# Performance work log

Hardware: AMD Instinct MI355X
Metric: run time of the kernel (lower is better)

## Reference

```python
import jax, jax.numpy as jnp
import numpy as np

DIM = 1024
DIM_HEAD = 64
HEADS = 8
MULT = 4
ATTN_INNER = HEADS * DIM_HEAD            # 512
FF_INNER = MULT * DIM                    # 4096
FUSED = ATTN_INNER + DIM_HEAD + DIM_HEAD + 2 * FF_INNER  # 8832


def setup_inputs() -> dict:
    key = jax.random.key(0)
    ks = jax.random.split(key, 5)
    x = jax.random.normal(ks[0], (2, 2048, DIM), dtype=jnp.float32)
    gamma = jnp.ones((DIM,), dtype=jnp.float32)
    # Linear weights stored as [in, out]
    w_fused = jax.random.normal(ks[1], (DIM, FUSED), dtype=jnp.float32) * (DIM ** -0.5)
    w_attn_out = jax.random.normal(ks[2], (ATTN_INNER, DIM), dtype=jnp.float32) * (ATTN_INNER ** -0.5)
    w_ff_out = jax.random.normal(ks[3], (FF_INNER, DIM), dtype=jnp.float32) * (FF_INNER ** -0.5)
    return {"x": x, "gamma": gamma, "w_fused": w_fused,
            "w_attn_out": w_attn_out, "w_ff_out": w_ff_out}


def _forward(x, gamma, w_fused, w_attn_out, w_ff_out):
    b, n, d = x.shape
    # LayerNorm (beta buffer is zeros)
    mu = jnp.mean(x, axis=-1, keepdims=True)
    var = jnp.mean(jnp.square(x - mu), axis=-1, keepdims=True)
    xn = (x - mu) * jax.lax.rsqrt(var + 1e-5) * gamma
    # fused QKV + FF projection
    proj = jnp.einsum('bnd,df->bnf', xn, w_fused)
    q = proj[..., :ATTN_INNER]
    k = proj[..., ATTN_INNER:ATTN_INNER + DIM_HEAD]
    v = proj[..., ATTN_INNER + DIM_HEAD:ATTN_INNER + 2 * DIM_HEAD]
    ff = proj[..., ATTN_INNER + 2 * DIM_HEAD:]
    # multi-query attention: single shared K/V head of width DIM_HEAD
    q = q.reshape(b, n, HEADS, DIM_HEAD).transpose(0, 2, 1, 3) * (DIM_HEAD ** -0.5)
    sim = jnp.einsum('bhid,bjd->bhij', q, k)
    attn = jax.nn.softmax(sim, axis=-1)
    out = jnp.einsum('bhij,bjd->bhid', attn, v)
    out = out.transpose(0, 2, 1, 3).reshape(b, n, ATTN_INNER)
    attn_out = jnp.einsum('bna,ad->bnd', out, w_attn_out)
    # parallel SwiGLU FF: chunk -> (x_part, gate); silu(gate)*x_part
    ff_x, gate = ff[..., :FF_INNER], ff[..., FF_INNER:]
    ff_out = jnp.einsum('bnf,fd->bnd', jax.nn.silu(gate) * ff_x, w_ff_out)
    return attn_out + ff_out


def reference(x, gamma, w_fused, w_attn_out, w_ff_out):
    return _forward(x, gamma, w_fused, w_attn_out, w_ff_out)
```

## Files before the change

### kernel.cpp

```cpp
#include <hip/hip_runtime.h>
#include <hip/hip_bf16.h>
#include <stdint.h>

#define DIM     1024
#define SEQ     2048
#define NTOK    4096
#define HEADS   8
#define DH      64
#define AINNER  512
#define FFI     4096
#define FUSED   8832
#define HCOLS   4608

typedef __attribute__((ext_vector_type(8))) short short8;
typedef __attribute__((ext_vector_type(4))) short short4v;
typedef __attribute__((ext_vector_type(4))) float f32x4;

__device__ __forceinline__ short f2bf(float f) {
  union { float f; uint32_t u; } v; v.f = f;
  uint32_t r = v.u + 0x7fffu + ((v.u >> 16) & 1u);
  return (short)(r >> 16);
}
__device__ __forceinline__ float bf2f(short s) {
  union { uint32_t u; float f; } v; v.u = ((uint32_t)(uint16_t)s) << 16;
  return v.f;
}
__device__ __forceinline__ void g2l16(const void* g, void* l) {
  __builtin_amdgcn_global_load_lds((const __attribute__((address_space(1))) void*)g,
                                   (__attribute__((address_space(3))) void*)l, 16, 0, 0);
}

__global__ __launch_bounds__(256) void k_transpose_wf(const float* __restrict__ src,
                                                      short* __restrict__ dst) {
  __shared__ short tile[32][33];
  int c0 = blockIdx.x * 32;
  int r0 = blockIdx.y * 32;
  int tx = threadIdx.x & 31, ty = threadIdx.x >> 5;
#pragma unroll
  for (int i = 0; i < 32; i += 8)
    tile[ty + i][tx] = f2bf(src[(size_t)(r0 + ty + i) * FUSED + c0 + tx]);
  __syncthreads();
#pragma unroll
  for (int i = 0; i < 32; i += 8)
    dst[(size_t)(c0 + ty + i) * DIM + r0 + tx] = tile[tx][ty + i];
}

__global__ __launch_bounds__(256) void k_transpose_w2(const float* __restrict__ wao,
                                                      const float* __restrict__ wfo,
                                                      short* __restrict__ dst) {
  __shared__ short tile[32][33];
  int c0 = blockIdx.x * 32;
  int r0 = blockIdx.y * 32;
  int tx = threadIdx.x & 31, ty = threadIdx.x >> 5;
#pragma unroll
  for (int i = 0; i < 32; i += 8) {
    int r = r0 + ty + i;
    float v = (r < AINNER) ? wao[(size_t)r * DIM + c0 + tx]
                           : wfo[(size_t)(r - AINNER) * DIM + c0 + tx];
    tile[ty + i][tx] = f2bf(v);
  }
  __syncthreads();
#pragma unroll
  for (int i = 0; i < 32; i += 8)
    dst[(size_t)(c0 + ty + i) * HCOLS + r0 + tx] = tile[tx][ty + i];
}

__global__ __launch_bounds__(256) void k_ln(const float* __restrict__ x,
                                            const float* __restrict__ gamma,
                                            short* __restrict__ xn) {
  int row = blockIdx.x;
  int t = threadIdx.x;
  const float4* xr = (const float4*)(x + (size_t)row * DIM);
  float4 v = xr[t];
  float s = v.x + v.y + v.z + v.w;
  float s2 = v.x * v.x + v.y * v.y + v.z * v.z + v.w * v.w;
#pragma unroll
  for (int m = 1; m < 64; m <<= 1) { s += __shfl_xor(s, m); s2 += __shfl_xor(s2, m); }
  __shared__ float red[8];
  int w = t >> 6;
  if ((t & 63) == 0) { red[w] = s; red[4 + w] = s2; }
  __syncthreads();
  s = red[0] + red[1] + red[2] + red[3];
  s2 = red[4] + red[5] + red[6] + red[7];
  float mu = s * (1.f / DIM);
  float rs = rsqrtf(s2 * (1.f / DIM) - mu * mu + 1e-5f);
  const float4* g4 = (const float4*)gamma;
  float4 g = g4[t];
  short4v o;
  o.x = f2bf((v.x - mu) * rs * g.x);
  o.y = f2bf((v.y - mu) * rs * g.y);
  o.z = f2bf((v.z - mu) * rs * g.z);
  o.w = f2bf((v.w - mu) * rs * g.w);
  ((short4v*)(xn + (size_t)row * DIM))[t] = o;
}

__global__ __launch_bounds__(512, 2) void p1(const short* __restrict__ A,
                                             const short* __restrict__ Bt,
                                             short* __restrict__ qb,
                                             short* __restrict__ kbf,
                                             short* __restrict__ vtb,
                                             short* __restrict__ H) {
  extern __shared__ __align__(16) short S[];
  int tid = threadIdx.x, l = tid & 63, w = tid >> 6;
  int wm = w >> 2, wn = w & 3;
  int hw = blockIdx.y * 37 + blockIdx.x;
  int tile = (hw & 7) * 74 + (hw >> 3);
  int bx = tile % 37, by = tile / 37;
  int mBase = by * 256;
  bool fused = bx < 32;
  int b0row = fused ? (640 + bx * 128) : ((bx - 32) * 128);
  int b1row = 4736 + bx * 128;

  int srow = w * 8 + (l >> 3);
  int cs = (l & 7) ^ (l >> 3);
  const short* Ag = A + (size_t)(mBase + srow) * DIM + cs * 8;
  const short* Bg0 = Bt + (size_t)(b0row + srow) * DIM + cs * 8;
  const short* Bg1 = Bt + (size_t)(b1row + srow) * DIM + cs * 8;
  int dsto = w * 512 + l * 8;

#define P1_STAGE(kt, db)                                                        \
  {                                                                             \
    _Pragma("unroll") for (int i = 0; i < 4; ++i)                               \
        g2l16(Ag + (size_t)(i * 64) * DIM + (kt) * 64,                          \
              S + (db) * 16384 + i * 4096 + dsto);                              \
    _Pragma("unroll") for (int i = 0; i < 2; ++i)                               \
        g2l16(Bg0 + (size_t)(i * 64) * DIM + (kt) * 64,                         \
              S + 32768 + (db) * 16384 + i * 4096 + dsto);                      \
    if (fused) {                                                                \
      _Pragma("unroll") for (int i = 0; i < 2; ++i)                             \
          g2l16(Bg1 + (size_t)(i * 64) * DIM + (kt) * 64,                       \
                S + 32768 + (db) * 16384 + 8192 + i * 4096 + dsto);             \
    }                                                                           \
  }

  const int NT = DIM / 64;
  P1_STAGE(0, 0);

  int c0 = l & 15, kg = l >> 4, cx = l & 7;
  f32x4 zero = {0.f, 0.f, 0.f, 0.f};
  f32x4 accF[8][2], accG[8][2];
#pragma unroll
  for (int m = 0; m < 8; ++m)
#pragma unroll
    for (int n = 0; n < 2; ++n) { accF[m][n] = zero; accG[m][n] = zero; }

  for (int kt = 0; kt < NT; ++kt) {
    int db = kt & 1, dbn = db ^ 1;
    asm volatile("s_waitcnt vmcnt(0)\ns_barrier" ::: "memory");
    if (kt + 1 < NT) P1_STAGE(kt + 1, dbn);
    const short* Ab = S + db * 16384;
    const short* Bb = S + 32768 + db * 16384;
#pragma unroll
    for (int kkh = 0; kkh < 2; ++kkh) {
      int ch8 = ((kkh * 4 + kg) ^ cx) * 8;
      short8 bf0 = *(const short8*)(Bb + (wn * 32 + c0) * 64 + ch8);
      short8 bf1 = *(const short8*)(Bb + (wn * 32 + 16 + c0) * 64 + ch8);
      if (fused) {
        short8 bg0 = *(const short8*)(Bb + (128 + wn * 32 + c0) * 64 + ch8);
        short8 bg1 = *(const short8*)(Bb + (128 + wn * 32 + 16 + c0) * 64 + ch8);
        __builtin_amdgcn_s_setprio(1);
#pragma unroll
        for (int m = 0; m < 8; ++m) {
          short8 a = *(const short8*)(Ab + (wm * 128 + m * 16 + c0) * 64 + ch8);
          accF[m][0] = __builtin_amdgcn_mfma_f32_16x16x32_bf16(a, bf0, accF[m][0], 0, 0, 0);
          accF[m][1] = __builtin_amdgcn_mfma_f32_16x16x32_bf16(a, bf1, accF[m][1], 0, 0, 0);
          accG[m][0] = __builtin_amdgcn_mfma_f32_16x16x32_bf16(a, bg0, accG[m][0], 0, 0, 0);
          accG[m][1] = __builtin_amdgcn_mfma_f32_16x16x32_bf16(a, bg1, accG[m][1], 0, 0, 0);
        }
        __builtin_amdgcn_s_setprio(0);
      } else {
        __builtin_amdgcn_s_setprio(1);
#pragma unroll
        for (int m = 0; m < 8; ++m) {
          short8 a = *(const short8*)(Ab + (wm * 128 + m * 16 + c0) * 64 + ch8);
          accF[m][0] = __builtin_amdgcn_mfma_f32_16x16x32_bf16(a, bf0, accF[m][0], 0, 0, 0);
          accF[m][1] = __builtin_amdgcn_mfma_f32_16x16x32_bf16(a, bf1, accF[m][1], 0, 0, 0);
        }
        __builtin_amdgcn_s_setprio(0);
      }
    }
  }
#undef P1_STAGE

  int r0 = (l >> 4) * 4;
#pragma unroll
  for (int m = 0; m < 8; ++m)
#pragma unroll
    for (int n = 0; n < 2; ++n)
#pragma unroll
      for (int r = 0; r < 4; ++r) {
        int row = mBase + wm * 128 + m * 16 + r0 + r;
        if (fused) {
          int col = bx * 128 + wn * 32 + n * 16 + c0;
          float g = accG[m][n][r];
          float sg = g / (1.f + __expf(-g));
          H[(size_t)row * HCOLS + AINNER + col] = f2bf(sg * accF[m][n][r]);
        } else {
          int col = (bx - 32) * 128 + wn * 32 + n * 16 + c0;
          float val = accF[m][n][r];
          if (col < AINNER)
            qb[(size_t)row * AINNER + col] = f2bf(val);
          else if (col < AINNER + DH)
            kbf[(size_t)row * DH + (col - AINNER)] = f2bf(val);
          else
            vtb[((size_t)(row >> 11) * DH + (col - AINNER - DH)) * SEQ +
                (row & (SEQ - 1))] = f2bf(val);
        }
      }
}

__global__ __launch_bounds__(512, 2) void gemm_s(const short* __restrict__ A,
                                                 const short* __restrict__ Bt,
                                                 short* __restrict__ part) {
  extern __shared__ __align__(16) short S[];
  int tid = threadIdx.x, l = tid & 63, w = tid >> 6;
  int wm = w >> 2, wn = w & 3;
  int hw = (blockIdx.z * 16 + blockIdx.y) * 4 + blockIdx.x;
  int tile = (hw & 7) * 32 + (hw >> 3);
  int bx = tile & 3, by = (tile >> 2) & 15, bz = tile >> 6;
  int mBase = by * 256, nBase = bx * 256;
  int kOff = bz * 1152;

  int srow = w * 8 + (l >> 3);
  int cs = (l & 7) ^ (l >> 3);
  const short* Ag = A + (size_t)(mBase + srow) * HCOLS + kOff + cs * 8;
  const short* Bg = Bt + (size_t)(nBase + srow) * HCOLS + kOff + cs * 8;
  int dsto = w * 512 + l * 8;

#define GS_STAGE(kt, db)                                                        \
  {                                                                             \
    _Pragma("unroll") for (int i = 0; i < 4; ++i) {                             \
      g2l16(Ag + (size_t)(i * 64) * HCOLS + (kt) * 64,                          \
            S + (db) * 16384 + i * 4096 + dsto);                                \
      g2l16(Bg + (size_t)(i * 64) * HCOLS + (kt) * 64,                          \
            S + 32768 + (db) * 16384 + i * 4096 + dsto);                        \
    }                                                                           \
  }

  const int NT = 18;
  GS_STAGE(0, 0);

  int c0 = l & 15, kg = l >> 4, cx = l & 7;
  f32x4 zero = {0.f, 0.f, 0.f, 0.f};
  f32x4 acc[8][4];
#pragma unroll
  for (int m = 0; m < 8; ++m)
#pragma unroll
    for (int n = 0; n < 4; ++n) acc[m][n] = zero;

  for (int kt = 0; kt < NT; ++kt) {
    int db = kt & 1, dbn = db ^ 1;
    asm volatile("s_waitcnt vmcnt(0)\ns_barrier" ::: "memory");
    if (kt + 1 < NT) GS_STAGE(kt + 1, dbn);
    const short* Ab = S + db * 16384;
    const short* Bb = S + 32768 + db * 16384;
#pragma unroll
    for (int kkh = 0; kkh < 2; ++kkh) {
      int ch8 = ((kkh * 4 + kg) ^ cx) * 8;
      short8 b[4];
#pragma unroll
      for (int n = 0; n < 4; ++n)
        b[n] = *(const short8*)(Bb + (wn * 64 + n * 16 + c0) * 64 + ch8);
      __builtin_amdgcn_s_setprio(1);
#pragma unroll
      for (int m = 0; m < 8; ++m) {
        short8 a = *(const short8*)(Ab + (wm * 128 + m * 16 + c0) * 64 + ch8);
#pragma unroll
        for (int n = 0; n < 4; ++n)
          acc[m][n] = __builtin_amdgcn_mfma_f32_16x16x32_bf16(a, b[n], acc[m][n], 0, 0, 0);
      }
      __builtin_amdgcn_s_setprio(0);
    }
  }
#undef GS_STAGE

  int r0 = (l >> 4) * 4;
#pragma unroll
  for (int m = 0; m < 8; ++m)
#pragma unroll
    for (int n = 0; n < 4; ++n)
#pragma unroll
      for (int r = 0; r < 4; ++r) {
        int row = mBase + wm * 128 + m * 16 + r0 + r;
        int col = nBase + wn * 64 + n * 16 + c0;
        part[(size_t)bz * (NTOK * DIM) + (size_t)row * DIM + col] = f2bf(acc[m][n][r]);
      }
}

__global__ __launch_bounds__(256) void k_red(const short* __restrict__ part,
                                             float* __restrict__ out) {
  int i = (blockIdx.x * 256 + threadIdx.x) * 4;
  float4 s = {0.f, 0.f, 0.f, 0.f};
#pragma unroll
  for (int ks = 0; ks < 4; ++ks) {
    short4v v = *(const short4v*)(part + (size_t)ks * (NTOK * DIM) + i);
    s.x += bf2f(v.x); s.y += bf2f(v.y); s.z += bf2f(v.z); s.w += bf2f(v.w);
  }
  *(float4*)(out + i) = s;
}

__global__ __launch_bounds__(512, 2) void gemm_r(const short* __restrict__ A, int lda,
                                                 const short* __restrict__ Bt, int ldb,
                                                 int K, float* __restrict__ out0) {
  extern __shared__ __align__(16) short SA[];
  int tid = threadIdx.x, l = tid & 63, w = tid >> 6;
  int gx = gridDim.x;
  int nwg = gx * gridDim.y;
  int hw = blockIdx.y * gx + blockIdx.x;
  int qq = nwg >> 3;
  int tile = (hw & 7) * qq + (hw >> 3);
  int bx = tile % gx, by = tile / gx;
  int mBase = by * 128, nBase = bx * 128;

  int srow = w * 8 + (l >> 3);
  int cs = (l & 7) ^ (l >> 3);
  const short* Ag = A + (size_t)(mBase + srow) * lda + cs * 8;
  const short* Bg = Bt + (size_t)(nBase + srow) * ldb + cs * 8;
  short* ldsA = SA + w * 512 + l * 8;
  short* ldsB = ldsA + 8192;

  int NT = K >> 6;
  for (int tt = 0; tt < 3; ++tt) {
    int slot = tt & 3;
#pragma unroll
    for (int i = 0; i < 2; ++i) {
      g2l16(Ag + (size_t)(i * 64) * lda + tt * 64, ldsA + slot * 16384 + i * 4096);
      g2l16(Bg + (size_t)(i * 64) * ldb + tt * 64, ldsB + slot * 16384 + i * 4096);
    }
  }

  int wr = w >> 2, wc = w & 3;
  int c0 = l & 15, kg = l >> 4, cx = l & 7;
  f32x4 zero = {0.f, 0.f, 0.f, 0.f};
  f32x4 acc[4][2];
#pragma unroll
  for (int m = 0; m < 4; ++m)
#pragma unroll
    for (int n = 0; n < 2; ++n) acc[m][n] = zero;

  for (int kt = 0; kt < NT; ++kt) {
    if (kt + 2 < NT)      asm volatile("s_waitcnt vmcnt(8)\ns_barrier" ::: "memory");
    else if (kt + 1 < NT) asm volatile("s_waitcnt vmcnt(4)\ns_barrier" ::: "memory");
    else                  asm volatile("s_waitcnt vmcnt(0)\ns_barrier" ::: "memory");
    int slot = kt & 3;
    const short* Ab = SA + slot * 16384;
    const short* Bb = Ab + 8192;
    short8 af[4][2], bfr[2][2];
#pragma unroll
    for (int m = 0; m < 4; ++m)
#pragma unroll
      for (int kk = 0; kk < 2; ++kk)
        af[m][kk] = *(const short8*)(Ab + (wr * 64 + m * 16 + c0) * 64 + ((kk * 4 + kg) ^ cx) * 8);
#pragma unroll
    for (int n = 0; n < 2; ++n)
#pragma unroll
      for (int kk = 0; kk < 2; ++kk)
        bfr[n][kk] = *(const short8*)(Bb + (wc * 32 + n * 16 + c0) * 64 + ((kk * 4 + kg) ^ cx) * 8);
    int ts = kt + 3;
    if (ts < NT) {
      int s2 = ts & 3;
#pragma unroll
      for (int i = 0; i < 2; ++i) {
        g2l16(Ag + (size_t)(i * 64) * lda + ts * 64, ldsA + s2 * 16384 + i * 4096);
        g2l16(Bg + (size_t)(i * 64) * ldb + ts * 64, ldsB + s2 * 16384 + i * 4096);
      }
    }
    __builtin_amdgcn_s_setprio(1);
#pragma unroll
    for (int m = 0; m < 4; ++m)
#pragma unroll
      for (int n = 0; n < 2; ++n)
#pragma unroll
        for (int kk = 0; kk < 2; ++kk)
          acc[m][n] = __builtin_amdgcn_mfma_f32_16x16x32_bf16(af[m][kk], bfr[n][kk],
                                                              acc[m][n], 0, 0, 0);
    __builtin_amdgcn_s_setprio(0);
  }

  int r0 = (l >> 4) * 4;
#pragma unroll
  for (int m = 0; m < 4; ++m)
#pragma unroll
    for (int n = 0; n < 2; ++n)
#pragma unroll
      for (int r = 0; r < 4; ++r) {
        int row = mBase + wr * 64 + m * 16 + r0 + r;
        int col = nBase + wc * 32 + n * 16 + c0;
        out0[(size_t)row * DIM + col] = acc[m][n][r];
      }
}

__global__ __launch_bounds__(256) void k_attn(const short* __restrict__ qb,
                                              const short* __restrict__ kb,
                                              const short* __restrict__ vt,
                                              short* __restrict__ H) {
  __shared__ __align__(16) short Qs[64 * 64];
  __shared__ __align__(16) short Ks[128 * 64];
  __shared__ __align__(16) short Vs[64 * 128];
  __shared__ __align__(16) short Ps[4][16 * 128];
  int t = threadIdx.x, l = t & 63, w = t >> 6;
  int qt = blockIdx.x, bh = blockIdx.y;
  int b = bh >> 3, h = bh & 7;
  int q0 = qt * 64;

  int srow = w * 8 + (l >> 3);
  int schunk = (l & 7) ^ (l >> 3);
  {
    const short* Qg = qb + (size_t)(b * SEQ + q0 + srow) * AINNER + h * DH + schunk * 8;
    short* qs = Qs + w * 512 + l * 8;
#pragma unroll
    for (int i = 0; i < 2; ++i) g2l16(Qg + (size_t)(i * 32) * AINNER, qs + i * 2048);
  }
  const short* Kg = kb + (size_t)(b * SEQ + srow) * DH + schunk * 8;
  short* ksl = Ks + w * 512 + l * 8;
  int vrow = w * 4 + (l >> 4);
  int vchunk = (l & 15) ^ (vrow & 7);
  const short* Vg = vt + (size_t)b * DH * SEQ + (size_t)vrow * SEQ + vchunk * 8;
  short* vsl = Vs + w * 512 + l * 8;

#pragma unroll
  for (int i = 0; i < 4; ++i) {
    g2l16(Kg + (size_t)(i * 32) * DH, ksl + i * 2048);
    g2l16(Vg + (size_t)(i * 16) * SEQ, vsl + i * 2048);
  }

  float m_run[4], l_run[4];
  f32x4 zero = {0.f, 0.f, 0.f, 0.f};
  f32x4 Oacc[4];
#pragma unroll
  for (int r = 0; r < 4; ++r) { m_run[r] = -1e30f; l_run[r] = 0.f; }
#pragma unroll
  for (int n = 0; n < 4; ++n) Oacc[n] = zero;

  int c0 = l & 15, kg = l >> 4, cx = l & 7;
  short* pw = Ps[w];

  for (int kv0 = 0; kv0 < SEQ; kv0 += 128) {
    asm volatile("s_waitcnt vmcnt(0)\ns_barrier" ::: "memory");

    f32x4 sacc[8];
#pragma unroll
    for (int n = 0; n < 8; ++n) sacc[n] = zero;
#pragma unroll
    for (int kk = 0; kk < 2; ++kk) {
      int rr = w * 16 + c0;
      short8 aq = *(const short8*)(Qs + rr * 64 + ((kk * 4 + kg) ^ cx) * 8);
#pragma unroll
      for (int n = 0; n < 8; ++n) {
        int kr = n * 16 + c0;
        short8 bk = *(const short8*)(Ks + kr * 64 + ((kk * 4 + kg) ^ cx) * 8);
        sacc[n] = __builtin_amdgcn_mfma_f32_16x16x32_bf16(aq, bk, sacc[n], 0, 0, 0);
      }
    }
#pragma unroll
    for (int r = 0; r < 4; ++r) {
      float mx = -1e30f;
#pragma unroll
      for (int n = 0; n < 8; ++n) {
        sacc[n][r] *= 0.125f;
        mx = fmaxf(mx, sacc[n][r]);
      }
#pragma unroll
      for (int msk = 1; msk < 16; msk <<= 1) mx = fmaxf(mx, __shfl_xor(mx, msk));
      float nm = fmaxf(m_run[r], mx);
      float corr = __expf(m_run[r] - nm);
      m_run[r] = nm;
      float rs = 0.f;
#pragma unroll
      for (int n = 0; n < 8; ++n) {
        float p = __expf(sacc[n][r] - nm);
        sacc[n][r] = p;
        rs += p;
      }
#pragma unroll
      for (int msk = 1; msk < 16; msk <<= 1) rs += __shfl_xor(rs, msk);
      l_run[r] = l_run[r] * corr + rs;
      Oacc[0][r] *= corr; Oacc[1][r] *= corr; Oacc[2][r] *= corr; Oacc[3][r] *= corr;
    }
#pragma unroll
    for (int n = 0; n < 8; ++n)
#pragma unroll
      for (int r = 0; r < 4; ++r) {
        int pr = (l >> 4) * 4 + r;
        int pc = n * 16 + c0;
        pw[pr * 128 + ((pc >> 3) ^ (pr & 7)) * 8 + (pc & 7)] = f2bf(sacc[n][r]);
      }
    asm volatile("s_waitcnt lgkmcnt(0)" ::: "memory");
#pragma unroll
    for (int kk = 0; kk < 4; ++kk) {
      int pr = c0;
      short8 ap = *(const short8*)(pw + pr * 128 + ((kk * 4 + kg) ^ cx) * 8);
#pragma unroll
      for (int n = 0; n < 4; ++n) {
        int vr = n * 16 + c0;
        short8 bv = *(const short8*)(Vs + vr * 128 + ((kk * 4 + kg) ^ (vr & 7)) * 8);
        Oacc[n] = __builtin_amdgcn_mfma_f32_16x16x32_bf16(ap, bv, Oacc[n], 0, 0, 0);
      }
    }
    __syncthreads();
    int nx = kv0 + 128;
    if (nx < SEQ) {
#pragma unroll
      for (int i = 0; i < 4; ++i) {
        g2l16(Kg + (size_t)(nx + i * 32) * DH, ksl + i * 2048);
        g2l16(Vg + nx + (size_t)(i * 16) * SEQ, vsl + i * 2048);
      }
    }
  }
#pragma unroll
  for (int r = 0; r < 4; ++r) {
    float inv = 1.f / l_run[r];
    int row = b * SEQ + q0 + w * 16 + (l >> 4) * 4 + r;
#pragma unroll
    for (int n = 0; n < 4; ++n) {
      int col = h * DH + n * 16 + c0;
      H[(size_t)row * HCOLS + col] = f2bf(Oacc[n][r] * inv);
    }
  }
}

extern "C" void kernel_launch(void* const* d_in, const int* in_sizes, int n_in,
                              void* d_out, int out_size, void* d_ws, size_t ws_size,
                              hipStream_t stream) {
  const float* x     = (const float*)d_in[0];
  const float* gamma = (const float*)d_in[1];
  const float* w_f   = (const float*)d_in[2];
  const float* w_ao  = (const float*)d_in[3];
  const float* w_fo  = (const float*)d_in[4];
  float* out = (float*)d_out;

  char* ws = (char*)d_ws;
  size_t o = 0;
  short* WtF = (short*)(ws + o); o += (size_t)FUSED * DIM * 2;
  short* Wt2 = (short*)(ws + o); o += (size_t)DIM * HCOLS * 2;
  short* xn  = (short*)(ws + o); o += (size_t)NTOK * DIM * 2;
  short* qb  = (short*)(ws + o); o += (size_t)NTOK * AINNER * 2;
  short* kbf = (short*)(ws + o); o += (size_t)NTOK * DH * 2;
  short* vtb = (short*)(ws + o); o += (size_t)NTOK * DH * 2;
  short* H   = (short*)(ws + o); o += (size_t)NTOK * HCOLS * 2;
  short* part = (short*)(ws + o);
  size_t need = o + (size_t)4 * NTOK * DIM * 2;

  k_transpose_wf<<<dim3(FUSED / 32, DIM / 32), 256, 0, stream>>>(w_f, WtF);
  k_transpose_w2<<<dim3(DIM / 32, HCOLS / 32), 256, 0, stream>>>(w_ao, w_fo, Wt2);
  k_ln<<<NTOK, 256, 0, stream>>>(x, gamma, xn);
  p1<<<dim3(37, 16), 512, 131072, stream>>>(xn, WtF, qb, kbf, vtb, H);
  k_attn<<<dim3(32, 16), 256, 0, stream>>>(qb, kbf, vtb, H);
  if (ws_size >= need) {
    gemm_s<<<dim3(4, 16, 4), 512, 131072, stream>>>(H, Wt2, part);
    k_red<<<NTOK * DIM / 1024, 256, 0, stream>>>(part, out);
  } else {
    gemm_r<<<dim3(8, 32), 512, 131072, stream>>>(H, HCOLS, Wt2, HCOLS, HCOLS, out);
  }
}
```

Baseline: 223.4 us.

## Use 4-wave blocks with larger per-wave tiles in projection and split-K GEMMs

Both the fused projection GEMM and the split-K output GEMM drop from 8 waves of 512 threads to 4 waves of 256 threads. Each wave now computes a larger output tile (up to 128x128 per wave), which raises register reuse of LDS fragments and cuts LDS read traffic per MFMA. The tile scheduler is remapped so fused and QKV tiles are interleaved per XCD chunk. The fallback gemm_r path and the workspace size check are removed, and the reduction kernel is widened to 8 elements per thread. The risks are much higher VGPR/AGPR pressure and lower occupancy, which could cause spills or leave global-load latency exposed.

```diff
diff --git a/kernel.cpp b/kernel.cpp
--- a/kernel.cpp
+++ b/kernel.cpp
@@ -29,6 +29,8 @@
   __builtin_amdgcn_global_load_lds((const __attribute__((address_space(1))) void*)g,
                                    (__attribute__((address_space(3))) void*)l, 16, 0, 0);
 }
+
+#define PH_W0 asm volatile("s_waitcnt vmcnt(0)\ns_barrier" ::: "memory")
 
 __global__ __launch_bounds__(256) void k_transpose_wf(const float* __restrict__ src,
                                                       short* __restrict__ dst) {
@@ -94,7 +96,7 @@
   ((short4v*)(xn + (size_t)row * DIM))[t] = o;
 }
 
-__global__ __launch_bounds__(512, 2) void p1(const short* __restrict__ A,
+__global__ __launch_bounds__(256, 1) void p1(const short* __restrict__ A,
                                              const short* __restrict__ Bt,
                                              short* __restrict__ qb,
                                              short* __restrict__ kbf,
@@ -102,12 +104,14 @@
                                              short* __restrict__ H) {
   extern __shared__ __align__(16) short S[];
   int tid = threadIdx.x, l = tid & 63, w = tid >> 6;
-  int wm = w >> 2, wn = w & 3;
   int hw = blockIdx.y * 37 + blockIdx.x;
   int tile = (hw & 7) * 74 + (hw >> 3);
-  int bx = tile % 37, by = tile / 37;
+  int c = tile / 74, j = tile % 74;
+  bool fused = j < 64;
+  int bx, by;
+  if (fused) { int f = c * 64 + j; by = f >> 5; bx = f & 31; }
+  else       { int q = c * 10 + (j - 64); by = q / 5; bx = 32 + q % 5; }
   int mBase = by * 256;
-  bool fused = bx < 32;
   int b0row = fused ? (640 + bx * 128) : ((bx - 32) * 128);
   int b1row = 4736 + bx * 128;
 
@@ -120,84 +124,115 @@
 
 #define P1_STAGE(kt, db)                                                        \
   {                                                                             \
+    _Pragma("unroll") for (int i = 0; i < 8; ++i)                               \
+        g2l16(Ag + (size_t)(i * 32) * DIM + (kt) * 64,                          \
+              S + (db) * 16384 + i * 2048 + dsto);                              \
     _Pragma("unroll") for (int i = 0; i < 4; ++i)                               \
-        g2l16(Ag + (size_t)(i * 64) * DIM + (kt) * 64,                          \
-              S + (db) * 16384 + i * 4096 + dsto);                              \
-    _Pragma("unroll") for (int i = 0; i < 2; ++i)                               \
-        g2l16(Bg0 + (size_t)(i * 64) * DIM + (kt) * 64,                         \
-              S + 32768 + (db) * 16384 + i * 4096 + dsto);                      \
+        g2l16(Bg0 + (size_t)(i * 32) * DIM + (kt) * 64,                         \
+              S + 32768 + (db) * 16384 + i * 2048 + dsto);                      \
     if (fused) {                                                                \
-      _Pragma("unroll") for (int i = 0; i < 2; ++i)                             \
-          g2l16(Bg1 + (size_t)(i * 64) * DIM + (kt) * 64,                       \
-                S + 32768 + (db) * 16384 + 8192 + i * 4096 + dsto);             \
+      _Pragma("unroll") for (int i = 0; i < 4; ++i)                             \
+          g2l16(Bg1 + (size_t)(i * 32) * DIM + (kt) * 64,                       \
+                S + 32768 + (db) * 16384 + 8192 + i * 2048 + dsto);             \
     }                                                                           \
   }
 
   const int NT = DIM / 64;
+  int c0 = l & 15, kg = l >> 4, cx = l & 7;
+  int r0 = (l >> 4) * 4;
+  int wm = w >> 1, wn = w & 1;
+  int ra = wm * 128, rbF = wn * 64, rbG = 128 + wn * 64;
+  f32x4 zero = {0.f, 0.f, 0.f, 0.f};
+
   P1_STAGE(0, 0);
 
-  int c0 = l & 15, kg = l >> 4, cx = l & 7;
-  f32x4 zero = {0.f, 0.f, 0.f, 0.f};
-  f32x4 accF[8][2], accG[8][2];
-#pragma unroll
-  for (int m = 0; m < 8; ++m)
-#pragma unroll
-    for (int n = 0; n < 2; ++n) { accF[m][n] = zero; accG[m][n] = zero; }
-
-  for (int kt = 0; kt < NT; ++kt) {
-    int db = kt & 1, dbn = db ^ 1;
-    asm volatile("s_waitcnt vmcnt(0)\ns_barrier" ::: "memory");
-    if (kt + 1 < NT) P1_STAGE(kt + 1, dbn);
-    const short* Ab = S + db * 16384;
-    const short* Bb = S + 32768 + db * 16384;
-#pragma unroll
-    for (int kkh = 0; kkh < 2; ++kkh) {
-      int ch8 = ((kkh * 4 + kg) ^ cx) * 8;
-      short8 bf0 = *(const short8*)(Bb + (wn * 32 + c0) * 64 + ch8);
-      short8 bf1 = *(const short8*)(Bb + (wn * 32 + 16 + c0) * 64 + ch8);
-      if (fused) {
-        short8 bg0 = *(const short8*)(Bb + (128 + wn * 32 + c0) * 64 + ch8);
-        short8 bg1 = *(const short8*)(Bb + (128 + wn * 32 + 16 + c0) * 64 + ch8);
+  if (fused) {
+    f32x4 accF[8][4], accG[8][4];
+#pragma unroll
+    for (int m = 0; m < 8; ++m)
+#pragma unroll
+      for (int n = 0; n < 4; ++n) { accF[m][n] = zero; accG[m][n] = zero; }
+    for (int kt = 0; kt < NT; ++kt) {
+      int db = kt & 1, dbn = db ^ 1;
+      PH_W0;
+      if (kt + 1 < NT) P1_STAGE(kt + 1, dbn);
+      const short* Ab = S + db * 16384;
+      const short* Bb = S + 32768 + db * 16384;
+#pragma unroll
+      for (int kk = 0; kk < 2; ++kk) {
+        int ch = ((kk * 4 + kg) ^ cx) * 8;
+        short8 a[8], bf[4], bg[4];
+#pragma unroll
+        for (int m = 0; m < 8; ++m)
+          a[m] = *(const short8*)(Ab + (ra + m * 16 + c0) * 64 + ch);
+#pragma unroll
+        for (int n = 0; n < 4; ++n) {
+          bf[n] = *(const short8*)(Bb + (rbF + n * 16 + c0) * 64 + ch);
+          bg[n] = *(const short8*)(Bb + (rbG + n * 16 + c0) * 64 + ch);
+        }
         __builtin_amdgcn_s_setprio(1);
 #pragma unroll
-        for (int m = 0; m < 8; ++m) {
-          short8 a = *(const short8*)(Ab + (wm * 128 + m * 16 + c0) * 64 + ch8);
-          accF[m][0] = __builtin_amdgcn_mfma_f32_16x16x32_bf16(a, bf0, accF[m][0], 0, 0, 0);
-          accF[m][1] = __builtin_amdgcn_mfma_f32_16x16x32_bf16(a, bf1, accF[m][1], 0, 0, 0);
-          accG[m][0] = __builtin_amdgcn_mfma_f32_16x16x32_bf16(a, bg0, accG[m][0], 0, 0, 0);
-          accG[m][1] = __builtin_amdgcn_mfma_f32_16x16x32_bf16(a, bg1, accG[m][1], 0, 0, 0);
-        }
+        for (int m = 0; m < 8; ++m)
+#pragma unroll
+          for (int n = 0; n < 4; ++n) {
+            accF[m][n] = __builtin_amdgcn_mfma_f32_16x16x32_bf16(a[m], bf[n], accF[m][n], 0, 0, 0);
+            accG[m][n] = __builtin_amdgcn_mfma_f32_16x16x32_bf16(a[m], bg[n], accG[m][n], 0, 0, 0);
+          }
         __builtin_amdgcn_s_setprio(0);
-      } else {
-        __builtin_amdgcn_s_setprio(1);
-#pragma unroll
-        for (int m = 0; m < 8; ++m) {
-          short8 a = *(const short8*)(Ab + (wm * 128 + m * 16 + c0) * 64 + ch8);
-          accF[m][0] = __builtin_amdgcn_mfma_f32_16x16x32_bf16(a, bf0, accF[m][0], 0, 0, 0);
-          accF[m][1] = __builtin_amdgcn_mfma_f32_16x16x32_bf16(a, bf1, accF[m][1], 0, 0, 0);
-        }
-        __builtin_amdgcn_s_setprio(0);
-      }
-    }
-  }
-#undef P1_STAGE
-
-  int r0 = (l >> 4) * 4;
-#pragma unroll
-  for (int m = 0; m < 8; ++m)
-#pragma unroll
-    for (int n = 0; n < 2; ++n)
-#pragma unroll
-      for (int r = 0; r < 4; ++r) {
-        int row = mBase + wm * 128 + m * 16 + r0 + r;
-        if (fused) {
-          int col = bx * 128 + wn * 32 + n * 16 + c0;
+      }
+    }
+#pragma unroll
+    for (int m = 0; m < 8; ++m)
+#pragma unroll
+      for (int n = 0; n < 4; ++n)
+#pragma unroll
+        for (int r = 0; r < 4; ++r) {
+          int row = mBase + ra + m * 16 + r0 + r;
+          int col = bx * 128 + wn * 64 + n * 16 + c0;
           float g = accG[m][n][r];
           float sg = g / (1.f + __expf(-g));
           H[(size_t)row * HCOLS + AINNER + col] = f2bf(sg * accF[m][n][r]);
-        } else {
-          int col = (bx - 32) * 128 + wn * 32 + n * 16 + c0;
-          float val = accF[m][n][r];
+        }
+  } else {
+    f32x4 acc[8][4];
+#pragma unroll
+    for (int m = 0; m < 8; ++m)
+#pragma unroll
+      for (int n = 0; n < 4; ++n) acc[m][n] = zero;
+    for (int kt = 0; kt < NT; ++kt) {
+      int db = kt & 1, dbn = db ^ 1;
+      PH_W0;
+      if (kt + 1 < NT) P1_STAGE(kt + 1, dbn);
+      const short* Ab = S + db * 16384;
+      const short* Bb = S + 32768 + db * 16384;
+#pragma unroll
+      for (int kk = 0; kk < 2; ++kk) {
+        int ch = ((kk * 4 + kg) ^ cx) * 8;
+        short8 a[8], b[4];
+#pragma unroll
+        for (int m = 0; m < 8; ++m)
+          a[m] = *(const short8*)(Ab + (ra + m * 16 + c0) * 64 + ch);
+#pragma unroll
+        for (int n = 0; n < 4; ++n)
+          b[n] = *(const short8*)(Bb + (rbF + n * 16 + c0) * 64 + ch);
+        __builtin_amdgcn_s_setprio(1);
+#pragma unroll
+        for (int m = 0; m < 8; ++m)
+#pragma unroll
+          for (int n = 0; n < 4; ++n)
+            acc[m][n] = __builtin_amdgcn_mfma_f32_16x16x32_bf16(a[m], b[n], acc[m][n], 0, 0, 0);
+        __builtin_amdgcn_s_setprio(0);
+      }
+    }
+#pragma unroll
+    for (int m = 0; m < 8; ++m)
+#pragma unroll
+      for (int n = 0; n < 4; ++n)
+#pragma unroll
+        for (int r = 0; r < 4; ++r) {
+          float val = acc[m][n][r];
+          int row = mBase + ra + m * 16 + r0 + r;
+          int col = (bx - 32) * 128 + wn * 64 + n * 16 + c0;
           if (col < AINNER)
             qb[(size_t)row * AINNER + col] = f2bf(val);
           else if (col < AINNER + DH)
@@ -206,15 +241,15 @@
             vtb[((size_t)(row >> 11) * DH + (col - AINNER - DH)) * SEQ +
                 (row & (SEQ - 1))] = f2bf(val);
         }
-      }
-}
-
-__global__ __launch_bounds__(512, 2) void gemm_s(const short* __restrict__ A,
+  }
+#undef P1_STAGE
+}
+
+__global__ __launch_bounds__(256, 1) void gemm_s(const short* __restrict__ A,
                                                  const short* __restrict__ Bt,
                                                  short* __restrict__ part) {
   extern __shared__ __align__(16) short S[];
   int tid = threadIdx.x, l = tid & 63, w = tid >> 6;
-  int wm = w >> 2, wn = w & 3;
   int hw = (blockIdx.z * 16 + blockIdx.y) * 4 + blockIdx.x;
   int tile = (hw & 7) * 32 + (hw >> 3);
   int bx = tile & 3, by = (tile >> 2) & 15, bz = tile >> 6;
@@ -229,11 +264,11 @@
 
 #define GS_STAGE(kt, db)                                                        \
   {                                                                             \
-    _Pragma("unroll") for (int i = 0; i < 4; ++i) {                             \
-      g2l16(Ag + (size_t)(i * 64) * HCOLS + (kt) * 64,                          \
-            S + (db) * 16384 + i * 4096 + dsto);                                \
-      g2l16(Bg + (size_t)(i * 64) * HCOLS + (kt) * 64,                          \
-            S + 32768 + (db) * 16384 + i * 4096 + dsto);                        \
+    _Pragma("unroll") for (int i = 0; i < 8; ++i) {                             \
+      g2l16(Ag + (size_t)(i * 32) * HCOLS + (kt) * 64,                          \
+            S + (db) * 16384 + i * 2048 + dsto);                                \
+      g2l16(Bg + (size_t)(i * 32) * HCOLS + (kt) * 64,                          \
+            S + 32768 + (db) * 16384 + i * 2048 + dsto);                        \
     }                                                                           \
   }
 
@@ -241,34 +276,36 @@
   GS_STAGE(0, 0);
 
   int c0 = l & 15, kg = l >> 4, cx = l & 7;
+  int ra = (w >> 1) * 128, rb = (w & 1) * 128;
   f32x4 zero = {0.f, 0.f, 0.f, 0.f};
-  f32x4 acc[8][4];
+  f32x4 acc[8][8];
 #pragma unroll
   for (int m = 0; m < 8; ++m)
 #pragma unroll
-    for (int n = 0; n < 4; ++n) acc[m][n] = zero;
+    for (int n = 0; n < 8; ++n) acc[m][n] = zero;
 
   for (int kt = 0; kt < NT; ++kt) {
     int db = kt & 1, dbn = db ^ 1;
-    asm volatile("s_waitcnt vmcnt(0)\ns_barrier" ::: "memory");
+    PH_W0;
     if (kt + 1 < NT) GS_STAGE(kt + 1, dbn);
     const short* Ab = S + db * 16384;
     const short* Bb = S + 32768 + db * 16384;
 #pragma unroll
-    for (int kkh = 0; kkh < 2; ++kkh) {
-      int ch8 = ((kkh * 4 + kg) ^ cx) * 8;
-      short8 b[4];
-#pragma unroll
-      for (int n = 0; n < 4; ++n)
-        b[n] = *(const short8*)(Bb + (wn * 64 + n * 16 + c0) * 64 + ch8);
+    for (int kk = 0; kk < 2; ++kk) {
+      int ch = ((kk * 4 + kg) ^ cx) * 8;
+      short8 a[8], b[8];
+#pragma unroll
+      for (int m = 0; m < 8; ++m)
+        a[m] = *(const short8*)(Ab + (ra + m * 16 + c0) * 64 + ch);
+#pragma unroll
+      for (int n = 0; n < 8; ++n)
+        b[n] = *(const short8*)(Bb + (rb + n * 16 + c0) * 64 + ch);
       __builtin_amdgcn_s_setprio(1);
 #pragma unroll
-      for (int m = 0; m < 8; ++m) {
-        short8 a = *(const short8*)(Ab + (wm * 128 + m * 16 + c0) * 64 + ch8);
-#pragma unroll
-        for (int n = 0; n < 4; ++n)
-          acc[m][n] = __builtin_amdgcn_mfma_f32_16x16x32_bf16(a, b[n], acc[m][n], 0, 0, 0);
-      }
+      for (int m = 0; m < 8; ++m)
+#pragma unroll
+        for (int n = 0; n < 8; ++n)
+          acc[m][n] = __builtin_amdgcn_mfma_f32_16x16x32_bf16(a[m], b[n], acc[m][n], 0, 0, 0);
       __builtin_amdgcn_s_setprio(0);
     }
   }
@@ -278,116 +315,29 @@
 #pragma unroll
   for (int m = 0; m < 8; ++m)
 #pragma unroll
-    for (int n = 0; n < 4; ++n)
+    for (int n = 0; n < 8; ++n)
 #pragma unroll
       for (int r = 0; r < 4; ++r) {
-        int row = mBase + wm * 128 + m * 16 + r0 + r;
-        int col = nBase + wn * 64 + n * 16 + c0;
+        int row = mBase + ra + m * 16 + r0 + r;
+        int col = nBase + rb + n * 16 + c0;
         part[(size_t)bz * (NTOK * DIM) + (size_t)row * DIM + col] = f2bf(acc[m][n][r]);
       }
 }
 
 __global__ __launch_bounds__(256) void k_red(const short* __restrict__ part,
                                              float* __restrict__ out) {
-  int i = (blockIdx.x * 256 + threadIdx.x) * 4;
-  float4 s = {0.f, 0.f, 0.f, 0.f};
+  int i = (blockIdx.x * 256 + threadIdx.x) * 8;
+  float s[8] = {0.f, 0.f, 0.f, 0.f, 0.f, 0.f, 0.f, 0.f};
 #pragma unroll
   for (int ks = 0; ks < 4; ++ks) {
-    short4v v = *(const short4v*)(part + (size_t)ks * (NTOK * DIM) + i);
-    s.x += bf2f(v.x); s.y += bf2f(v.y); s.z += bf2f(v.z); s.w += bf2f(v.w);
-  }
-  *(float4*)(out + i) = s;
-}
-
-__global__ __launch_bounds__(512, 2) void gemm_r(const short* __restrict__ A, int lda,
-                                                 const short* __restrict__ Bt, int ldb,
-                                                 int K, float* __restrict__ out0) {
-  extern __shared__ __align__(16) short SA[];
-  int tid = threadIdx.x, l = tid & 63, w = tid >> 6;
-  int gx = gridDim.x;
-  int nwg = gx * gridDim.y;
-  int hw = blockIdx.y * gx + blockIdx.x;
-  int qq = nwg >> 3;
-  int tile = (hw & 7) * qq + (hw >> 3);
-  int bx = tile % gx, by = tile / gx;
-  int mBase = by * 128, nBase = bx * 128;
-
-  int srow = w * 8 + (l >> 3);
-  int cs = (l & 7) ^ (l >> 3);
-  const short* Ag = A + (size_t)(mBase + srow) * lda + cs * 8;
-  const short* Bg = Bt + (size_t)(nBase + srow) * ldb + cs * 8;
-  short* ldsA = SA + w * 512 + l * 8;
-  short* ldsB = ldsA + 8192;
-
-  int NT = K >> 6;
-  for (int tt = 0; tt < 3; ++tt) {
-    int slot = tt & 3;
-#pragma unroll
-    for (int i = 0; i < 2; ++i) {
-      g2l16(Ag + (size_t)(i * 64) * lda + tt * 64, ldsA + slot * 16384 + i * 4096);
-      g2l16(Bg + (size_t)(i * 64) * ldb + tt * 64, ldsB + slot * 16384 + i * 4096);
-    }
-  }
-
-  int wr = w >> 2, wc = w & 3;
-  int c0 = l & 15, kg = l >> 4, cx = l & 7;
-  f32x4 zero = {0.f, 0.f, 0.f, 0.f};
-  f32x4 acc[4][2];
-#pragma unroll
-  for (int m = 0; m < 4; ++m)
-#pragma unroll
-    for (int n = 0; n < 2; ++n) acc[m][n] = zero;
-
-  for (int kt = 0; kt < NT; ++kt) {
-    if (kt + 2 < NT)      asm volatile("s_waitcnt vmcnt(8)\ns_barrier" ::: "memory");
-    else if (kt + 1 < NT) asm volatile("s_waitcnt vmcnt(4)\ns_barrier" ::: "memory");
-    else                  asm volatile("s_waitcnt vmcnt(0)\ns_barrier" ::: "memory");
-    int slot = kt & 3;
-    const short* Ab = SA + slot * 16384;
-    const short* Bb = Ab + 8192;
-    short8 af[4][2], bfr[2][2];
-#pragma unroll
-    for (int m = 0; m < 4; ++m)
-#pragma unroll
-      for (int kk = 0; kk < 2; ++kk)
-        af[m][kk] = *(const short8*)(Ab + (wr * 64 + m * 16 + c0) * 64 + ((kk * 4 + kg) ^ cx) * 8);
-#pragma unroll
-    for (int n = 0; n < 2; ++n)
-#pragma unroll
-      for (int kk = 0; kk < 2; ++kk)
-        bfr[n][kk] = *(const short8*)(Bb + (wc * 32 + n * 16 + c0) * 64 + ((kk * 4 + kg) ^ cx) * 8);
-    int ts = kt + 3;
-    if (ts < NT) {
-      int s2 = ts & 3;
-#pragma unroll
-      for (int i = 0; i < 2; ++i) {
-        g2l16(Ag + (size_t)(i * 64) * lda + ts * 64, ldsA + s2 * 16384 + i * 4096);
-        g2l16(Bg + (size_t)(i * 64) * ldb + ts * 64, ldsB + s2 * 16384 + i * 4096);
-      }
-    }
-    __builtin_amdgcn_s_setprio(1);
-#pragma unroll
-    for (int m = 0; m < 4; ++m)
-#pragma unroll
-      for (int n = 0; n < 2; ++n)
-#pragma unroll
-        for (int kk = 0; kk < 2; ++kk)
-          acc[m][n] = __builtin_amdgcn_mfma_f32_16x16x32_bf16(af[m][kk], bfr[n][kk],
-                                                              acc[m][n], 0, 0, 0);
-    __builtin_amdgcn_s_setprio(0);
-  }
-
-  int r0 = (l >> 4) * 4;
-#pragma unroll
-  for (int m = 0; m < 4; ++m)
-#pragma unroll
-    for (int n = 0; n < 2; ++n)
-#pragma unroll
-      for (int r = 0; r < 4; ++r) {
-        int row = mBase + wr * 64 + m * 16 + r0 + r;
-        int col = nBase + wc * 32 + n * 16 + c0;
-        out0[(size_t)row * DIM + col] = acc[m][n][r];
-      }
+    short8 v = *(const short8*)(part + (size_t)ks * (NTOK * DIM) + i);
+#pragma unroll
+    for (int jj = 0; jj < 8; ++jj) s[jj] += bf2f(v[jj]);
+  }
+  float4 lo = {s[0], s[1], s[2], s[3]};
+  float4 hi = {s[4], s[5], s[6], s[7]};
+  *(float4*)(out + i) = lo;
+  *(float4*)(out + i + 4) = hi;
 }
 
 __global__ __launch_bounds__(256) void k_attn(const short* __restrict__ qb,
@@ -539,17 +489,12 @@
   short* vtb = (short*)(ws + o); o += (size_t)NTOK * DH * 2;
   short* H   = (short*)(ws + o); o += (size_t)NTOK * HCOLS * 2;
   short* part = (short*)(ws + o);
-  size_t need = o + (size_t)4 * NTOK * DIM * 2;
 
   k_transpose_wf<<<dim3(FUSED / 32, DIM / 32), 256, 0, stream>>>(w_f, WtF);
   k_transpose_w2<<<dim3(DIM / 32, HCOLS / 32), 256, 0, stream>>>(w_ao, w_fo, Wt2);
   k_ln<<<NTOK, 256, 0, stream>>>(x, gamma, xn);
-  p1<<<dim3(37, 16), 512, 131072, stream>>>(xn, WtF, qb, kbf, vtb, H);
+  p1<<<dim3(37, 16), 256, 131072, stream>>>(xn, WtF, qb, kbf, vtb, H);
   k_attn<<<dim3(32, 16), 256, 0, stream>>>(qb, kbf, vtb, H);
-  if (ws_size >= need) {
-    gemm_s<<<dim3(4, 16, 4), 512, 131072, stream>>>(H, Wt2, part);
-    k_red<<<NTOK * DIM / 1024, 256, 0, stream>>>(part, out);
-  } else {
-    gemm_r<<<dim3(8, 32), 512, 131072, stream>>>(H, HCOLS, Wt2, HCOLS, HCOLS, out);
-  }
-}
+  gemm_s<<<dim3(4, 16, 4), 256, 131072, stream>>>(H, Wt2, part);
+  k_red<<<NTOK * DIM / 2048, 256, 0, stream>>>(part, out);
+}
```

Result: no change. 227.4 us (+1.8%).
